# Kernel optimization log

Hardware: AMD Instinct MI355X
Metric: run time of the kernel (lower is better)

The kernel has to match this reference:

```python
import jax, jax.numpy as jnp
import numpy as np

N = 1024          # number of proposals
D_APP = 1024      # appearance_feature_dim
D_K = 64          # key_feature_dim
D_G = 64          # geo_feature_dim
NR = 16           # n_relations


def setup_inputs() -> dict:
    key = jax.random.key(0)
    ks = jax.random.split(key, 12)
    s = 0.02
    return {
        "f_a": jax.random.normal(ks[0], (N, D_APP), dtype=jnp.float32),
        "position_embedding": jax.random.uniform(ks[1], (N, N, D_G), dtype=jnp.float32),
        # stacked per-relation params; torch Linear weight layout [out, in]
        "WG_w": jax.random.normal(ks[2], (NR, D_G), dtype=jnp.float32) * s,
        "WG_b": jax.random.normal(ks[3], (NR,), dtype=jnp.float32) * s,
        "WK_w": jax.random.normal(ks[4], (NR, D_K, D_APP), dtype=jnp.float32) * s,
        "WK_b": jax.random.normal(ks[5], (NR, D_K), dtype=jnp.float32) * s,
        "WQ_w": jax.random.normal(ks[6], (NR, D_K, D_APP), dtype=jnp.float32) * s,
        "WQ_b": jax.random.normal(ks[7], (NR, D_K), dtype=jnp.float32) * s,
        "WV_w": jax.random.normal(ks[8], (NR, D_K, D_APP), dtype=jnp.float32) * s,
        "WV_b": jax.random.normal(ks[9], (NR, D_K), dtype=jnp.float32) * s,
    }


def reference(f_a, position_embedding, WG_w, WG_b, WK_w, WK_b, WQ_w, WQ_b, WV_w, WV_b):
    n = f_a.shape[0]
    # geometric gate: relu(Linear(pos_emb)) per relation -> [R, N, N]
    pe = position_embedding.reshape(-1, WG_w.shape[1])  # [N*N, D_G]
    w_g = jax.nn.relu(jnp.einsum('pg,rg->rp', pe, WG_w) + WG_b[:, None])
    w_g = w_g.reshape(WG_w.shape[0], n, n)
    # per-relation K/Q/V projections: [R, N, D_K]
    K = jnp.einsum('nf,rdf->rnd', f_a, WK_w) + WK_b[:, None, :]
    Q = jnp.einsum('nf,rdf->rnd', f_a, WQ_w) + WQ_b[:, None, :]
    V = jnp.einsum('nf,rdf->rnd', f_a, WV_w) + WV_b[:, None, :]
    dk = K.shape[-1]
    # note: row index n comes from K, column index m from Q (as in the torch code)
    scores = jnp.einsum('rnd,rmd->rnm', K, Q) / jnp.sqrt(jnp.asarray(dk, K.dtype))
    w_mn = jnp.log(jnp.clip(w_g, 1e-6)) + scores
    attn = jax.nn.softmax(w_mn, axis=2)  # softmax over m (dim=1 in torch NxN view)
    out = jnp.einsum('rnm,rmd->rnd', attn, V)  # [R, N, D_K]
    R, _, d = out.shape
    concat = jnp.transpose(out, (1, 0, 2)).reshape(n, R * d)  # [N, R*D_K]
    return concat + f_a
```

## Files before the change

### kernel.cpp

```cpp
#include <hip/hip_runtime.h>
#include <hip/hip_bf16.h>
#include <math.h>

#define NN 1024
#define DAPP 1024
#define DK 64
#define DG 64
#define NR 16

typedef __bf16 bf16x8 __attribute__((ext_vector_type(8)));
typedef float f32x4 __attribute__((ext_vector_type(4)));

static constexpr size_t OFF_FAB = 0;
static constexpr size_t OFF_WB  = OFF_FAB + (size_t)NN * DAPP * 2;
static constexpr size_t OFF_KB  = OFF_WB + (size_t)3 * NR * DK * DAPP * 2;
static constexpr size_t OFF_QB  = OFF_KB + (size_t)NR * NN * DK * 2;
static constexpr size_t OFF_V   = OFF_QB + (size_t)NR * NN * DK * 2;
static constexpr size_t OFF_S   = OFF_V + (size_t)NR * NN * DK * 4;
static constexpr size_t OFF_ST  = OFF_S + (size_t)NR * NN * NN * 4;

__global__ __launch_bounds__(256) void cast_kernel(
    const float* __restrict__ fa, const float* __restrict__ wk,
    const float* __restrict__ wq, const float* __restrict__ wv,
    __bf16* __restrict__ fab, __bf16* __restrict__ wb) {
  int i = blockIdx.x * 256 + threadIdx.x;
  const int M1 = NN * DAPP;
  if (i < M1) {
    fab[i] = (__bf16)fa[i];
  } else {
    int j = i - M1;
    int p = j >> 20;
    int o = j & (M1 - 1);
    const float* src = (p == 0) ? wk : ((p == 1) ? wq : wv);
    wb[j] = (__bf16)src[o];
  }
}

__global__ __launch_bounds__(256) void kqv_kernel(
    const __bf16* __restrict__ fab, const __bf16* __restrict__ wb,
    const float* __restrict__ kbias, const float* __restrict__ qbias,
    const float* __restrict__ vbias,
    __bf16* __restrict__ Kb, __bf16* __restrict__ Qb, float* __restrict__ V) {
  int wave = blockIdx.x * 4 + (threadIdx.x >> 6);
  int l = threadIdx.x & 63;
  int nt = wave / 96;
  int jt = wave % 96;
  int n0 = nt * 32, j0 = jt * 32;
  int ra = l & 15;
  int ko = (l >> 4) * 8;

  f32x4 acc[2][2] = {};
  for (int k0 = 0; k0 < DAPP; k0 += 32) {
    bf16x8 a0 = *(const bf16x8*)(fab + (size_t)(n0 + ra) * DAPP + k0 + ko);
    bf16x8 a1 = *(const bf16x8*)(fab + (size_t)(n0 + 16 + ra) * DAPP + k0 + ko);
    bf16x8 b0 = *(const bf16x8*)(wb + (size_t)(j0 + ra) * DAPP + k0 + ko);
    bf16x8 b1 = *(const bf16x8*)(wb + (size_t)(j0 + 16 + ra) * DAPP + k0 + ko);
    acc[0][0] = __builtin_amdgcn_mfma_f32_16x16x32_bf16(a0, b0, acc[0][0], 0, 0, 0);
    acc[0][1] = __builtin_amdgcn_mfma_f32_16x16x32_bf16(a0, b1, acc[0][1], 0, 0, 0);
    acc[1][0] = __builtin_amdgcn_mfma_f32_16x16x32_bf16(a1, b0, acc[1][0], 0, 0, 0);
    acc[1][1] = __builtin_amdgcn_mfma_f32_16x16x32_bf16(a1, b1, acc[1][1], 0, 0, 0);
  }

  #pragma unroll
  for (int i = 0; i < 2; i++) {
    #pragma unroll
    for (int jj = 0; jj < 2; jj++) {
      #pragma unroll
      for (int q = 0; q < 4; q++) {
        int n = n0 + i * 16 + (l >> 4) * 4 + q;
        int col = j0 + jj * 16 + (l & 15);
        int proj = col >> 10;
        int rd = col & 1023;
        int r = rd >> 6, d = rd & 63;
        float v = acc[i][jj][q];
        size_t oidx = ((size_t)r * NN + n) * DK + d;
        if (proj == 0)      Kb[oidx] = (__bf16)(v + kbias[rd]);
        else if (proj == 1) Qb[oidx] = (__bf16)(v + qbias[rd]);
        else                V[oidx] = v + vbias[rd];
      }
    }
  }
}

__global__ __launch_bounds__(256) void scores_kernel(
    const __bf16* __restrict__ Kb, const __bf16* __restrict__ Qb,
    float* __restrict__ S) {
  int wave = blockIdx.x * 4 + (threadIdx.x >> 6);
  int r = wave >> 10;
  int idx = wave & 1023;
  int n0 = (idx >> 5) * 32;
  int m0 = (idx & 31) * 32;
  int l = threadIdx.x & 63;
  int ra = l & 15;
  int ko = (l >> 4) * 8;
  const __bf16* Kr = Kb + (size_t)r * NN * DK;
  const __bf16* Qr = Qb + (size_t)r * NN * DK;

  f32x4 acc[2][2] = {};
  #pragma unroll
  for (int k0 = 0; k0 < DK; k0 += 32) {
    bf16x8 a0 = *(const bf16x8*)(Kr + (n0 + ra) * DK + k0 + ko);
    bf16x8 a1 = *(const bf16x8*)(Kr + (n0 + 16 + ra) * DK + k0 + ko);
    bf16x8 b0 = *(const bf16x8*)(Qr + (m0 + ra) * DK + k0 + ko);
    bf16x8 b1 = *(const bf16x8*)(Qr + (m0 + 16 + ra) * DK + k0 + ko);
    acc[0][0] = __builtin_amdgcn_mfma_f32_16x16x32_bf16(a0, b0, acc[0][0], 0, 0, 0);
    acc[0][1] = __builtin_amdgcn_mfma_f32_16x16x32_bf16(a0, b1, acc[0][1], 0, 0, 0);
    acc[1][0] = __builtin_amdgcn_mfma_f32_16x16x32_bf16(a1, b0, acc[1][0], 0, 0, 0);
    acc[1][1] = __builtin_amdgcn_mfma_f32_16x16x32_bf16(a1, b1, acc[1][1], 0, 0, 0);
  }

  #pragma unroll
  for (int i = 0; i < 2; i++) {
    #pragma unroll
    for (int jj = 0; jj < 2; jj++) {
      #pragma unroll
      for (int q = 0; q < 4; q++) {
        int n = n0 + i * 16 + (l >> 4) * 4 + q;
        int m = m0 + jj * 16 + (l & 15);
        S[((size_t)r * NN + n) * NN + m] = acc[i][jj][q] * 0.125f;
      }
    }
  }
}

__global__ __launch_bounds__(256) void gate_kernel(
    const float* __restrict__ pe, const float* __restrict__ WGw,
    const float* __restrict__ WGb, float* __restrict__ S) {
  __shared__ float4 wgt[16][16];
  __shared__ float wgb[16];
  int t = threadIdx.x;
  {
    int g4 = t >> 4, r = t & 15;
    wgt[g4][r] = ((const float4*)WGw)[r * 16 + g4];
    if (t < 16) wgb[t] = WGb[t];
  }
  __syncthreads();

  int n = blockIdx.x >> 2;
  int m = ((blockIdx.x & 3) << 8) + t;
  const float4* pe4 = (const float4*)(pe + ((size_t)n * NN + m) * DG);

  float acc[16];
  #pragma unroll
  for (int r = 0; r < 16; r++) acc[r] = wgb[r];

  #pragma unroll
  for (int g4 = 0; g4 < 16; g4++) {
    float4 p = pe4[g4];
    #pragma unroll
    for (int r = 0; r < 16; r++) {
      float4 w = wgt[g4][r];
      acc[r] += p.x * w.x + p.y * w.y + p.z * w.z + p.w * w.w;
    }
  }

  size_t base = (size_t)n * NN + m;
  #pragma unroll
  for (int r = 0; r < 16; r++) {
    float lg = __logf(fmaxf(acc[r], 1e-6f));
    size_t idx = (size_t)r * NN * NN + base;
    S[idx] += lg;
  }
}

__global__ __launch_bounds__(256) void stats_kernel(
    const float* __restrict__ S, float2* __restrict__ stats) {
  int row = blockIdx.x * 4 + (threadIdx.x >> 6);
  int l = threadIdx.x & 63;
  const float* Sp = S + (size_t)row * NN;
  float v[16];
  float mx = -1e30f;
  #pragma unroll
  for (int i = 0; i < 16; i++) {
    v[i] = Sp[l + 64 * i];
    mx = fmaxf(mx, v[i]);
  }
  #pragma unroll
  for (int off = 32; off >= 1; off >>= 1) mx = fmaxf(mx, __shfl_xor(mx, off, 64));
  float sm = 0.f;
  #pragma unroll
  for (int i = 0; i < 16; i++) sm += __expf(v[i] - mx);
  #pragma unroll
  for (int off = 32; off >= 1; off >>= 1) sm += __shfl_xor(sm, off, 64);
  if (l == 0) stats[row] = make_float2(mx, sm);
}

__global__ __launch_bounds__(256) void pv_kernel(
    const float* __restrict__ S, const float2* __restrict__ stats,
    const float* __restrict__ V, const float* __restrict__ fa,
    float* __restrict__ out) {
  int r = blockIdx.x >> 5;
  int n0 = (blockIdx.x & 31) * 32;
  __shared__ float Pt[64][36];
  __shared__ float Vt[64][68];
  __shared__ float2 st[32];
  int t = threadIdx.x;
  if (t < 32) st[t] = stats[r * NN + n0 + t];

  int d0 = (t & 15) * 4;
  int nl0 = (t >> 4) * 2;
  float acc[2][4] = {};

  for (int m0 = 0; m0 < NN; m0 += 64) {
    __syncthreads();
    {
      int nl = t >> 3;
      int ml = (t & 7) * 8;
      const float* sp = S + ((size_t)r * NN + n0 + nl) * NN + m0 + ml;
      float mxn = st[nl].x;
      #pragma unroll
      for (int u = 0; u < 8; u++) Pt[ml + u][nl] = __expf(sp[u] - mxn);
    }
    {
      int ml = t >> 2;
      int dq = (t & 3) * 16;
      const float* vp = V + ((size_t)r * NN + m0 + ml) * DK + dq;
      #pragma unroll
      for (int u = 0; u < 4; u++) {
        float4 vv = ((const float4*)vp)[u];
        *(float4*)&Vt[ml][dq + u * 4] = vv;
      }
    }
    __syncthreads();
    #pragma unroll 8
    for (int ml = 0; ml < 64; ml++) {
      float a0 = Pt[ml][nl0];
      float a1 = Pt[ml][nl0 + 1];
      float4 vv = *(const float4*)&Vt[ml][d0];
      acc[0][0] += a0 * vv.x; acc[0][1] += a0 * vv.y;
      acc[0][2] += a0 * vv.z; acc[0][3] += a0 * vv.w;
      acc[1][0] += a1 * vv.x; acc[1][1] += a1 * vv.y;
      acc[1][2] += a1 * vv.z; acc[1][3] += a1 * vv.w;
    }
  }

  #pragma unroll
  for (int i = 0; i < 2; i++) {
    int n = n0 + nl0 + i;
    float rs = 1.0f / st[nl0 + i].y;
    int col = r * DK + d0;
    const float4 f = *(const float4*)(fa + (size_t)n * DAPP + col);
    float4 o;
    o.x = acc[i][0] * rs + f.x;
    o.y = acc[i][1] * rs + f.y;
    o.z = acc[i][2] * rs + f.z;
    o.w = acc[i][3] * rs + f.w;
    *(float4*)(out + (size_t)n * DAPP + col) = o;
  }
}

extern "C" void kernel_launch(void* const* d_in, const int* in_sizes, int n_in,
                              void* d_out, int out_size, void* d_ws, size_t ws_size,
                              hipStream_t stream) {
  const float* fa  = (const float*)d_in[0];
  const float* pe  = (const float*)d_in[1];
  const float* WGw = (const float*)d_in[2];
  const float* WGb = (const float*)d_in[3];
  const float* WKw = (const float*)d_in[4];
  const float* WKb = (const float*)d_in[5];
  const float* WQw = (const float*)d_in[6];
  const float* WQb = (const float*)d_in[7];
  const float* WVw = (const float*)d_in[8];
  const float* WVb = (const float*)d_in[9];
  float* out = (float*)d_out;

  char* ws = (char*)d_ws;
  __bf16* fab = (__bf16*)(ws + OFF_FAB);
  __bf16* wb  = (__bf16*)(ws + OFF_WB);
  __bf16* Kb  = (__bf16*)(ws + OFF_KB);
  __bf16* Qb  = (__bf16*)(ws + OFF_QB);
  float*  V   = (float*)(ws + OFF_V);
  float*  S   = (float*)(ws + OFF_S);
  float2* st  = (float2*)(ws + OFF_ST);

  cast_kernel<<<(4 * NN * DAPP / (NN * DAPP)) * (NN * DAPP / 256) , 256, 0, stream>>>(
      fa, WKw, WQw, WVw, fab, wb);
  kqv_kernel<<<768, 256, 0, stream>>>(fab, wb, WKb, WQb, WVb, Kb, Qb, V);
  scores_kernel<<<4096, 256, 0, stream>>>(Kb, Qb, S);
  gate_kernel<<<4096, 256, 0, stream>>>(pe, WGw, WGb, S);
  stats_kernel<<<4096, 256, 0, stream>>>(S, st);
  pv_kernel<<<512, 256, 0, stream>>>(S, st, V, fa, out);
}
```

Measured before the change: 560.3 us.

## Store score matrix in fp16 and fuse gate with online softmax stats

The score buffer S is now stored as half precision, halving its write and read traffic across the scores, gate and pv kernels. The gate kernel is merged with the stats kernel. Each thread keeps per-relation running max/sum (online softmax) over four column chunks, and the partial stats are combined with wave shuffles and shared memory, which removes one full pass over S. The risks are fp16 precision loss in the logits and fewer blocks (1024) in the fused kernel, which do more serial work each.

```diff
diff --git a/kernel.cpp b/kernel.cpp
--- a/kernel.cpp
+++ b/kernel.cpp
@@ -1,5 +1,6 @@
 #include <hip/hip_runtime.h>
 #include <hip/hip_bf16.h>
+#include <hip/hip_fp16.h>
 #include <math.h>
 
 #define NN 1024
@@ -9,6 +10,7 @@
 #define NR 16
 
 typedef __bf16 bf16x8 __attribute__((ext_vector_type(8)));
+typedef _Float16 f16x8 __attribute__((ext_vector_type(8)));
 typedef float f32x4 __attribute__((ext_vector_type(4)));
 
 static constexpr size_t OFF_FAB = 0;
@@ -17,7 +19,7 @@
 static constexpr size_t OFF_QB  = OFF_KB + (size_t)NR * NN * DK * 2;
 static constexpr size_t OFF_V   = OFF_QB + (size_t)NR * NN * DK * 2;
 static constexpr size_t OFF_S   = OFF_V + (size_t)NR * NN * DK * 4;
-static constexpr size_t OFF_ST  = OFF_S + (size_t)NR * NN * NN * 4;
+static constexpr size_t OFF_ST  = OFF_S + (size_t)NR * NN * NN * 2;
 
 __global__ __launch_bounds__(256) void cast_kernel(
     const float* __restrict__ fa, const float* __restrict__ wk,
@@ -84,7 +86,7 @@
 
 __global__ __launch_bounds__(256) void scores_kernel(
     const __bf16* __restrict__ Kb, const __bf16* __restrict__ Qb,
-    float* __restrict__ S) {
+    _Float16* __restrict__ S) {
   int wave = blockIdx.x * 4 + (threadIdx.x >> 6);
   int r = wave >> 10;
   int idx = wave & 1023;
@@ -117,17 +119,19 @@
       for (int q = 0; q < 4; q++) {
         int n = n0 + i * 16 + (l >> 4) * 4 + q;
         int m = m0 + jj * 16 + (l & 15);
-        S[((size_t)r * NN + n) * NN + m] = acc[i][jj][q] * 0.125f;
-      }
-    }
-  }
-}
-
-__global__ __launch_bounds__(256) void gate_kernel(
+        S[((size_t)r << 20) + ((size_t)n << 10) + m] = (_Float16)(acc[i][jj][q] * 0.125f);
+      }
+    }
+  }
+}
+
+__global__ __launch_bounds__(256) void gate_stats_kernel(
     const float* __restrict__ pe, const float* __restrict__ WGw,
-    const float* __restrict__ WGb, float* __restrict__ S) {
+    const float* __restrict__ WGb, _Float16* __restrict__ S,
+    float2* __restrict__ stats) {
   __shared__ float4 wgt[16][16];
   __shared__ float wgb[16];
+  __shared__ float2 red[16][4];
   int t = threadIdx.x;
   {
     int g4 = t >> 4, r = t & 15;
@@ -136,57 +140,68 @@
   }
   __syncthreads();
 
-  int n = blockIdx.x >> 2;
-  int m = ((blockIdx.x & 3) << 8) + t;
-  const float4* pe4 = (const float4*)(pe + ((size_t)n * NN + m) * DG);
-
-  float acc[16];
-  #pragma unroll
-  for (int r = 0; r < 16; r++) acc[r] = wgb[r];
-
-  #pragma unroll
-  for (int g4 = 0; g4 < 16; g4++) {
-    float4 p = pe4[g4];
+  int n = blockIdx.x;
+  float mx[16], lsum[16];
+  #pragma unroll
+  for (int r = 0; r < 16; r++) { mx[r] = -1e30f; lsum[r] = 0.f; }
+
+  for (int c = 0; c < 4; c++) {
+    int m = c * 256 + t;
+    const float4* pe4 = (const float4*)(pe + (((size_t)n << 10) + m) * DG);
+    float acc[16];
+    #pragma unroll
+    for (int r = 0; r < 16; r++) acc[r] = wgb[r];
+    #pragma unroll
+    for (int g4 = 0; g4 < 16; g4++) {
+      float4 p = pe4[g4];
+      #pragma unroll
+      for (int r = 0; r < 16; r++) {
+        float4 w = wgt[g4][r];
+        acc[r] += p.x * w.x + p.y * w.y + p.z * w.z + p.w * w.w;
+      }
+    }
+    size_t base = ((size_t)n << 10) + m;
     #pragma unroll
     for (int r = 0; r < 16; r++) {
-      float4 w = wgt[g4][r];
-      acc[r] += p.x * w.x + p.y * w.y + p.z * w.z + p.w * w.w;
-    }
-  }
-
-  size_t base = (size_t)n * NN + m;
+      size_t idx = ((size_t)r << 20) + base;
+      float v = (float)S[idx] + __logf(fmaxf(acc[r], 1e-6f));
+      S[idx] = (_Float16)v;
+      float nm = fmaxf(mx[r], v);
+      lsum[r] = lsum[r] * __expf(mx[r] - nm) + __expf(v - nm);
+      mx[r] = nm;
+    }
+  }
+
+  int lane = t & 63, wave = t >> 6;
   #pragma unroll
   for (int r = 0; r < 16; r++) {
-    float lg = __logf(fmaxf(acc[r], 1e-6f));
-    size_t idx = (size_t)r * NN * NN + base;
-    S[idx] += lg;
-  }
-}
-
-__global__ __launch_bounds__(256) void stats_kernel(
-    const float* __restrict__ S, float2* __restrict__ stats) {
-  int row = blockIdx.x * 4 + (threadIdx.x >> 6);
-  int l = threadIdx.x & 63;
-  const float* Sp = S + (size_t)row * NN;
-  float v[16];
-  float mx = -1e30f;
-  #pragma unroll
-  for (int i = 0; i < 16; i++) {
-    v[i] = Sp[l + 64 * i];
-    mx = fmaxf(mx, v[i]);
-  }
-  #pragma unroll
-  for (int off = 32; off >= 1; off >>= 1) mx = fmaxf(mx, __shfl_xor(mx, off, 64));
-  float sm = 0.f;
-  #pragma unroll
-  for (int i = 0; i < 16; i++) sm += __expf(v[i] - mx);
-  #pragma unroll
-  for (int off = 32; off >= 1; off >>= 1) sm += __shfl_xor(sm, off, 64);
-  if (l == 0) stats[row] = make_float2(mx, sm);
+    float m_ = mx[r], l_ = lsum[r];
+    #pragma unroll
+    for (int off = 1; off <= 32; off <<= 1) {
+      float om = __shfl_xor(m_, off, 64);
+      float ol = __shfl_xor(l_, off, 64);
+      float nm = fmaxf(m_, om);
+      l_ = l_ * __expf(m_ - nm) + ol * __expf(om - nm);
+      m_ = nm;
+    }
+    if (lane == 0) red[r][wave] = make_float2(m_, l_);
+  }
+  __syncthreads();
+  if (t < 16) {
+    float2 a = red[t][0];
+    #pragma unroll
+    for (int w = 1; w < 4; w++) {
+      float2 b = red[t][w];
+      float nm = fmaxf(a.x, b.x);
+      a.y = a.y * __expf(a.x - nm) + b.y * __expf(b.x - nm);
+      a.x = nm;
+    }
+    stats[(t << 10) + n] = a;
+  }
 }
 
 __global__ __launch_bounds__(256) void pv_kernel(
-    const float* __restrict__ S, const float2* __restrict__ stats,
+    const _Float16* __restrict__ S, const float2* __restrict__ stats,
     const float* __restrict__ V, const float* __restrict__ fa,
     float* __restrict__ out) {
   int r = blockIdx.x >> 5;
@@ -206,10 +221,11 @@
     {
       int nl = t >> 3;
       int ml = (t & 7) * 8;
-      const float* sp = S + ((size_t)r * NN + n0 + nl) * NN + m0 + ml;
+      const _Float16* sp = S + ((size_t)r << 20) + ((size_t)(n0 + nl) << 10) + m0 + ml;
+      f16x8 sv = *(const f16x8*)sp;
       float mxn = st[nl].x;
       #pragma unroll
-      for (int u = 0; u < 8; u++) Pt[ml + u][nl] = __expf(sp[u] - mxn);
+      for (int u = 0; u < 8; u++) Pt[ml + u][nl] = __expf((float)sv[u] - mxn);
     }
     {
       int ml = t >> 2;
@@ -270,14 +286,12 @@
   __bf16* Kb  = (__bf16*)(ws + OFF_KB);
   __bf16* Qb  = (__bf16*)(ws + OFF_QB);
   float*  V   = (float*)(ws + OFF_V);
-  float*  S   = (float*)(ws + OFF_S);
+  _Float16* S = (_Float16*)(ws + OFF_S);
   float2* st  = (float2*)(ws + OFF_ST);
 
-  cast_kernel<<<(4 * NN * DAPP / (NN * DAPP)) * (NN * DAPP / 256) , 256, 0, stream>>>(
-      fa, WKw, WQw, WVw, fab, wb);
+  cast_kernel<<<16384, 256, 0, stream>>>(fa, WKw, WQw, WVw, fab, wb);
   kqv_kernel<<<768, 256, 0, stream>>>(fab, wb, WKb, WQb, WVb, Kb, Qb, V);
   scores_kernel<<<4096, 256, 0, stream>>>(Kb, Qb, S);
-  gate_kernel<<<4096, 256, 0, stream>>>(pe, WGw, WGb, S);
-  stats_kernel<<<4096, 256, 0, stream>>>(S, st);
+  gate_stats_kernel<<<1024, 256, 0, stream>>>(pe, WGw, WGb, S, st);
   pv_kernel<<<512, 256, 0, stream>>>(S, st, V, fa, out);
 }
```

After: 677.3 us. +20.9%, slower.

## Fuse gate and score kernels and store logits in fp16

Applied to the files above, without the earlier changes.

Merges the geometric gate computation and the K·Q score MFMA into one kernel that writes the combined logits once, as fp16, instead of writing fp32 scores and then doing a read-modify-write pass. The stats and PV kernels now read half-size fp16 logits with vector loads. This removes a full fp32 round trip over the 64 MB score tensor. The cost is fp16 precision on the logits and a grid of only 512 blocks for the fused kernel.

```diff
diff --git a/kernel.cpp b/kernel.cpp
--- a/kernel.cpp
+++ b/kernel.cpp
@@ -1,5 +1,6 @@
 #include <hip/hip_runtime.h>
 #include <hip/hip_bf16.h>
+#include <hip/hip_fp16.h>
 #include <math.h>
 
 #define NN 1024
@@ -9,6 +10,8 @@
 #define NR 16
 
 typedef __bf16 bf16x8 __attribute__((ext_vector_type(8)));
+typedef _Float16 f16x8 __attribute__((ext_vector_type(8)));
+typedef _Float16 f16x4 __attribute__((ext_vector_type(4)));
 typedef float f32x4 __attribute__((ext_vector_type(4)));
 
 static constexpr size_t OFF_FAB = 0;
@@ -17,7 +20,7 @@
 static constexpr size_t OFF_QB  = OFF_KB + (size_t)NR * NN * DK * 2;
 static constexpr size_t OFF_V   = OFF_QB + (size_t)NR * NN * DK * 2;
 static constexpr size_t OFF_S   = OFF_V + (size_t)NR * NN * DK * 4;
-static constexpr size_t OFF_ST  = OFF_S + (size_t)NR * NN * NN * 4;
+static constexpr size_t OFF_ST  = OFF_S + (size_t)NR * NN * NN * 2;
 
 __global__ __launch_bounds__(256) void cast_kernel(
     const float* __restrict__ fa, const float* __restrict__ wk,
@@ -82,99 +85,95 @@
   }
 }
 
-__global__ __launch_bounds__(256) void scores_kernel(
+__global__ __launch_bounds__(256) void gate_score_kernel(
+    const float* __restrict__ pe, const float* __restrict__ WGw,
+    const float* __restrict__ WGb,
     const __bf16* __restrict__ Kb, const __bf16* __restrict__ Qb,
-    float* __restrict__ S) {
-  int wave = blockIdx.x * 4 + (threadIdx.x >> 6);
-  int r = wave >> 10;
-  int idx = wave & 1023;
-  int n0 = (idx >> 5) * 32;
-  int m0 = (idx & 31) * 32;
-  int l = threadIdx.x & 63;
-  int ra = l & 15;
-  int ko = (l >> 4) * 8;
-  const __bf16* Kr = Kb + (size_t)r * NN * DK;
-  const __bf16* Qr = Qb + (size_t)r * NN * DK;
-
-  f32x4 acc[2][2] = {};
-  #pragma unroll
-  for (int k0 = 0; k0 < DK; k0 += 32) {
-    bf16x8 a0 = *(const bf16x8*)(Kr + (n0 + ra) * DK + k0 + ko);
-    bf16x8 a1 = *(const bf16x8*)(Kr + (n0 + 16 + ra) * DK + k0 + ko);
-    bf16x8 b0 = *(const bf16x8*)(Qr + (m0 + ra) * DK + k0 + ko);
-    bf16x8 b1 = *(const bf16x8*)(Qr + (m0 + 16 + ra) * DK + k0 + ko);
-    acc[0][0] = __builtin_amdgcn_mfma_f32_16x16x32_bf16(a0, b0, acc[0][0], 0, 0, 0);
-    acc[0][1] = __builtin_amdgcn_mfma_f32_16x16x32_bf16(a0, b1, acc[0][1], 0, 0, 0);
-    acc[1][0] = __builtin_amdgcn_mfma_f32_16x16x32_bf16(a1, b0, acc[1][0], 0, 0, 0);
-    acc[1][1] = __builtin_amdgcn_mfma_f32_16x16x32_bf16(a1, b1, acc[1][1], 0, 0, 0);
-  }
-
-  #pragma unroll
-  for (int i = 0; i < 2; i++) {
-    #pragma unroll
-    for (int jj = 0; jj < 2; jj++) {
-      #pragma unroll
-      for (int q = 0; q < 4; q++) {
-        int n = n0 + i * 16 + (l >> 4) * 4 + q;
-        int m = m0 + jj * 16 + (l & 15);
-        S[((size_t)r * NN + n) * NN + m] = acc[i][jj][q] * 0.125f;
-      }
-    }
-  }
-}
-
-__global__ __launch_bounds__(256) void gate_kernel(
-    const float* __restrict__ pe, const float* __restrict__ WGw,
-    const float* __restrict__ WGb, float* __restrict__ S) {
+    _Float16* __restrict__ X) {
   __shared__ float4 wgt[16][16];
   __shared__ float wgb[16];
+  __shared__ _Float16 lg[16][16][36];
   int t = threadIdx.x;
+  int nt = blockIdx.x >> 3, mc = blockIdx.x & 7;
+  int n0 = nt * 16, m0 = mc * 128;
   {
     int g4 = t >> 4, r = t & 15;
     wgt[g4][r] = ((const float4*)WGw)[r * 16 + g4];
     if (t < 16) wgb[t] = WGb[t];
   }
+  int l = t & 63, w = t >> 6;
+  int rb = w * 4;
+  int ra = l & 15;
+  int ko = (l >> 4) * 8;
+
+  bf16x8 kf[4][2];
+  #pragma unroll
+  for (int rr = 0; rr < 4; rr++)
+    #pragma unroll
+    for (int kk = 0; kk < 2; kk++)
+      kf[rr][kk] = *(const bf16x8*)(Kb + (((size_t)(rb + rr) << 10) + n0 + ra) * DK + kk * 32 + ko);
   __syncthreads();
 
-  int n = blockIdx.x >> 2;
-  int m = ((blockIdx.x & 3) << 8) + t;
-  const float4* pe4 = (const float4*)(pe + ((size_t)n * NN + m) * DG);
-
-  float acc[16];
-  #pragma unroll
-  for (int r = 0; r < 16; r++) acc[r] = wgb[r];
-
-  #pragma unroll
-  for (int g4 = 0; g4 < 16; g4++) {
-    float4 p = pe4[g4];
-    #pragma unroll
-    for (int r = 0; r < 16; r++) {
-      float4 w = wgt[g4][r];
-      acc[r] += p.x * w.x + p.y * w.y + p.z * w.z + p.w * w.w;
-    }
-  }
-
-  size_t base = (size_t)n * NN + m;
-  #pragma unroll
-  for (int r = 0; r < 16; r++) {
-    float lg = __logf(fmaxf(acc[r], 1e-6f));
-    size_t idx = (size_t)r * NN * NN + base;
-    S[idx] += lg;
+  for (int ms = 0; ms < 4; ms++) {
+    #pragma unroll
+    for (int pp = 0; pp < 2; pp++) {
+      int p = t + pp * 256;
+      int n = p >> 5, ml = p & 31;
+      const float4* pe4 = (const float4*)(pe + (((size_t)(n0 + n) << 10) + m0 + ms * 32 + ml) * DG);
+      float acc[16];
+      #pragma unroll
+      for (int r = 0; r < 16; r++) acc[r] = wgb[r];
+      #pragma unroll
+      for (int g4 = 0; g4 < 16; g4++) {
+        float4 pv = pe4[g4];
+        #pragma unroll
+        for (int r = 0; r < 16; r++) {
+          float4 wv = wgt[g4][r];
+          acc[r] = fmaf(pv.x, wv.x, fmaf(pv.y, wv.y, fmaf(pv.z, wv.z, fmaf(pv.w, wv.w, acc[r]))));
+        }
+      }
+      #pragma unroll
+      for (int r = 0; r < 16; r++)
+        lg[r][n][ml] = (_Float16)__logf(fmaxf(acc[r], 1e-6f));
+    }
+    __syncthreads();
+    #pragma unroll
+    for (int rr = 0; rr < 4; rr++) {
+      int r = rb + rr;
+      const __bf16* Qr = Qb + (((size_t)r << 10)) * DK;
+      #pragma unroll
+      for (int mt = 0; mt < 2; mt++) {
+        int mbase = m0 + ms * 32 + mt * 16;
+        f32x4 acc2 = {};
+        #pragma unroll
+        for (int kk = 0; kk < 2; kk++) {
+          bf16x8 qa = *(const bf16x8*)(Qr + (size_t)(mbase + ra) * DK + kk * 32 + ko);
+          acc2 = __builtin_amdgcn_mfma_f32_16x16x32_bf16(qa, kf[rr][kk], acc2, 0, 0, 0);
+        }
+        f16x4 lgv = *(const f16x4*)&lg[r][ra][mt * 16 + ((l >> 4) << 2)];
+        f16x4 xv;
+        #pragma unroll
+        for (int q = 0; q < 4; q++)
+          xv[q] = (_Float16)(acc2[q] * 0.125f + (float)lgv[q]);
+        *(f16x4*)(X + ((size_t)r << 20) + ((size_t)(n0 + ra) << 10) + mbase + ((l >> 4) << 2)) = xv;
+      }
+    }
+    __syncthreads();
   }
 }
 
 __global__ __launch_bounds__(256) void stats_kernel(
-    const float* __restrict__ S, float2* __restrict__ stats) {
+    const _Float16* __restrict__ X, float2* __restrict__ stats) {
   int row = blockIdx.x * 4 + (threadIdx.x >> 6);
   int l = threadIdx.x & 63;
-  const float* Sp = S + (size_t)row * NN;
+  const f16x8* Sp = (const f16x8*)(X + ((size_t)row << 10) + l * 16);
+  f16x8 a = Sp[0], b = Sp[1];
   float v[16];
   float mx = -1e30f;
   #pragma unroll
-  for (int i = 0; i < 16; i++) {
-    v[i] = Sp[l + 64 * i];
-    mx = fmaxf(mx, v[i]);
-  }
+  for (int i = 0; i < 8; i++) { v[i] = (float)a[i]; v[8 + i] = (float)b[i]; }
+  #pragma unroll
+  for (int i = 0; i < 16; i++) mx = fmaxf(mx, v[i]);
   #pragma unroll
   for (int off = 32; off >= 1; off >>= 1) mx = fmaxf(mx, __shfl_xor(mx, off, 64));
   float sm = 0.f;
@@ -186,7 +185,7 @@
 }
 
 __global__ __launch_bounds__(256) void pv_kernel(
-    const float* __restrict__ S, const float2* __restrict__ stats,
+    const _Float16* __restrict__ S, const float2* __restrict__ stats,
     const float* __restrict__ V, const float* __restrict__ fa,
     float* __restrict__ out) {
   int r = blockIdx.x >> 5;
@@ -206,10 +205,11 @@
     {
       int nl = t >> 3;
       int ml = (t & 7) * 8;
-      const float* sp = S + ((size_t)r * NN + n0 + nl) * NN + m0 + ml;
+      const _Float16* sp = S + ((size_t)r << 20) + ((size_t)(n0 + nl) << 10) + m0 + ml;
+      f16x8 sv = *(const f16x8*)sp;
       float mxn = st[nl].x;
       #pragma unroll
-      for (int u = 0; u < 8; u++) Pt[ml + u][nl] = __expf(sp[u] - mxn);
+      for (int u = 0; u < 8; u++) Pt[ml + u][nl] = __expf((float)sv[u] - mxn);
     }
     {
       int ml = t >> 2;
@@ -270,14 +270,12 @@
   __bf16* Kb  = (__bf16*)(ws + OFF_KB);
   __bf16* Qb  = (__bf16*)(ws + OFF_QB);
   float*  V   = (float*)(ws + OFF_V);
-  float*  S   = (float*)(ws + OFF_S);
+  _Float16* X = (_Float16*)(ws + OFF_S);
   float2* st  = (float2*)(ws + OFF_ST);
 
-  cast_kernel<<<(4 * NN * DAPP / (NN * DAPP)) * (NN * DAPP / 256) , 256, 0, stream>>>(
-      fa, WKw, WQw, WVw, fab, wb);
+  cast_kernel<<<16384, 256, 0, stream>>>(fa, WKw, WQw, WVw, fab, wb);
   kqv_kernel<<<768, 256, 0, stream>>>(fab, wb, WKb, WQb, WVb, Kb, Qb, V);
-  scores_kernel<<<4096, 256, 0, stream>>>(Kb, Qb, S);
-  gate_kernel<<<4096, 256, 0, stream>>>(pe, WGw, WGb, S);
-  stats_kernel<<<4096, 256, 0, stream>>>(S, st);
-  pv_kernel<<<512, 256, 0, stream>>>(S, st, V, fa, out);
-}
+  gate_score_kernel<<<512, 256, 0, stream>>>(pe, WGw, WGb, Kb, Qb, X);
+  stats_kernel<<<4096, 256, 0, stream>>>(X, st);
+  pv_kernel<<<512, 256, 0, stream>>>(X, st, V, fa, out);
+}
```

Result: slower. 608.3 us (+8.6%).
